# Kernel tuning notes

Hardware: AMD Instinct MI355X
Metric: run time of the kernel (lower is better)

## Reference

```python
import jax, jax.numpy as jnp
import numpy as np

INV_SQRT2 = np.float32(2.0 ** -0.5)
EPS = 1e-5


def _bn5(x, g, b, m, v):
    # inference-mode BatchNorm3d over channel axis 1 of NCDHW
    r = (1, -1, 1, 1, 1)
    return (x - m.reshape(r)) * (g.reshape(r) * jax.lax.rsqrt(v.reshape(r) + EPS)) + b.reshape(r)


def _conv3d(x, w, b, dil=1, pad=0):
    out = jax.lax.conv_general_dilated(
        x, w, window_strides=(1, 1, 1), padding=[(pad, pad)] * 3,
        rhs_dilation=(dil, dil, dil),
        dimension_numbers=('NCDHW', 'OIDHW', 'NCDHW'))
    return out + b.reshape(1, -1, 1, 1, 1)


def _haar_dwt2(x):
    # pywt dwt2(x, 'haar', axes=(-3,-2)) for even-length axes.
    # axis -3 (D): a = approx, d = detail (pywt sign: (x0 - x1)/sqrt2)
    a = (x[:, :, 0::2] + x[:, :, 1::2]) * INV_SQRT2
    d = (x[:, :, 0::2] - x[:, :, 1::2]) * INV_SQRT2
    # axis -2 (H)
    LL = (a[:, :, :, 0::2] + a[:, :, :, 1::2]) * INV_SQRT2  # 'aa'
    HL = (a[:, :, :, 0::2] - a[:, :, :, 1::2]) * INV_SQRT2  # 'ad'
    LH = (d[:, :, :, 0::2] + d[:, :, :, 1::2]) * INV_SQRT2  # 'da'
    HH = (d[:, :, :, 0::2] - d[:, :, :, 1::2]) * INV_SQRT2  # 'dd'
    return LL, LH, HL, HH


def setup_inputs() -> dict:
    key = jax.random.key(0)
    ks = jax.random.split(key, 12)
    B, C1, D, H, W = 2, 60, 128, 128, 64
    CH, R = 64, 4  # gate channels, CH // reduction_ratio
    f32 = jnp.float32
    inp = {
        'x1': jax.random.normal(ks[0], (B, C1, D // 2, H // 2, W), f32),
        'x2': jax.random.normal(ks[1], (B, 1, D, H, W), f32),
        # BatchNorm3d(4) on dwt features
        'bn_g': jnp.ones(4, f32), 'bn_b': jnp.zeros(4, f32),
        'bn_m': jnp.zeros(4, f32), 'bn_v': jnp.ones(4, f32),
        # BAM channel gate: Linear(64->4), BN1d(4), Linear(4->64)
        'cg_w1': jax.random.normal(ks[2], (R, CH), f32) * 0.05,
        'cg_b1': jnp.zeros(R, f32),
        'cg_bng': jnp.ones(R, f32), 'cg_bnb': jnp.zeros(R, f32),
        'cg_bnm': jnp.zeros(R, f32), 'cg_bnv': jnp.ones(R, f32),
        'cg_w2': jax.random.normal(ks[3], (CH, R), f32) * 0.05,
        'cg_b2': jnp.zeros(CH, f32),
        # BAM spatial gate
        'sg_w0': jax.random.normal(ks[4], (R, CH, 1, 1, 1), f32) * 0.05,
        'sg_b0': jnp.zeros(R, f32),
        'sg_g0': jnp.ones(R, f32), 'sg_be0': jnp.zeros(R, f32),
        'sg_m0': jnp.zeros(R, f32), 'sg_v0': jnp.ones(R, f32),
        'sg_w1': jax.random.normal(ks[5], (R, R, 3, 3, 3), f32) * 0.05,
        'sg_b1': jnp.zeros(R, f32),
        'sg_g1': jnp.ones(R, f32), 'sg_be1': jnp.zeros(R, f32),
        'sg_m1': jnp.zeros(R, f32), 'sg_v1': jnp.ones(R, f32),
        'sg_w2': jax.random.normal(ks[6], (R, R, 3, 3, 3), f32) * 0.05,
        'sg_b2': jnp.zeros(R, f32),
        'sg_g2': jnp.ones(R, f32), 'sg_be2': jnp.zeros(R, f32),
        'sg_m2': jnp.zeros(R, f32), 'sg_v2': jnp.ones(R, f32),
        'sg_w3': jax.random.normal(ks[7], (1, R, 1, 1, 1), f32) * 0.05,
        'sg_b3': jnp.zeros(1, f32),
    }
    return inp


def reference(x1, x2, bn_g, bn_b, bn_m, bn_v,
              cg_w1, cg_b1, cg_bng, cg_bnb, cg_bnm, cg_bnv, cg_w2, cg_b2,
              sg_w0, sg_b0, sg_g0, sg_be0, sg_m0, sg_v0,
              sg_w1, sg_b1, sg_g1, sg_be1, sg_m1, sg_v1,
              sg_w2, sg_b2, sg_g2, sg_be2, sg_m2, sg_v2,
              sg_w3, sg_b3):
    LL, LH, HL, HH = _haar_dwt2(x2)
    dwt = jnp.concatenate([LL, LH, HL, HH], axis=1)          # [B,4,D/2,H/2,W]
    dwt = jax.nn.relu(_bn5(dwt, bn_g, bn_b, bn_m, bn_v))
    feat = jnp.concatenate([dwt, x1], axis=1)                # [B,64,D/2,H/2,W]

    # BAM channel gate
    pooled = feat.mean(axis=(2, 3, 4))                        # [B,64]
    h = pooled @ cg_w1.T + cg_b1
    h = jax.nn.relu((h - cg_bnm) * (cg_bng * jax.lax.rsqrt(cg_bnv + EPS)) + cg_bnb)
    att_c = (h @ cg_w2.T + cg_b2)[:, :, None, None, None]     # [B,64,1,1,1]

    # BAM spatial gate
    s = jax.nn.relu(_bn5(_conv3d(feat, sg_w0, sg_b0), sg_g0, sg_be0, sg_m0, sg_v0))
    s = jax.nn.relu(_bn5(_conv3d(s, sg_w1, sg_b1, dil=4, pad=4), sg_g1, sg_be1, sg_m1, sg_v1))
    s = jax.nn.relu(_bn5(_conv3d(s, sg_w2, sg_b2, dil=4, pad=4), sg_g2, sg_be2, sg_m2, sg_v2))
    att_s = _conv3d(s, sg_w3, sg_b3)                          # [B,1,D/2,H/2,W]

    scale = 1.0 + jax.nn.sigmoid(att_c + att_s)
    return (feat * scale, LL)
```

## Files before the change

kernel.cpp:

```cpp
#include <hip/hip_runtime.h>
#include <math.h>

#define EPSBN 1e-5f

typedef float f32x2 __attribute__((ext_vector_type(2)));
typedef float f32x4 __attribute__((ext_vector_type(4)));

constexpr int B   = 2;
constexpr int C1  = 60;
constexpr int NV  = 64 * 64 * 64;
constexpr int NBa = NV / 512;

__global__ __launch_bounds__(256) void kA(
    const float* __restrict__ x1, const float* __restrict__ x2,
    const float* __restrict__ bn_g, const float* __restrict__ bn_b,
    const float* __restrict__ bn_m, const float* __restrict__ bn_v,
    const float* __restrict__ sg_w0, const float* __restrict__ sg_b0,
    const float* __restrict__ sg_g0, const float* __restrict__ sg_be0,
    const float* __restrict__ sg_m0, const float* __restrict__ sg_v0,
    float* __restrict__ dwtM, float* __restrict__ s0,
    float* __restrict__ part, float* __restrict__ outLL)
{
    __shared__ float wsumq[64][65];

    const int tid = threadIdx.x;
    const int qid = tid >> 2;

    float dsc[4], dsh[4], c0A[4], c0B[4];
    #pragma unroll
    for (int r = 0; r < 4; ++r) {
        float d = bn_g[r] * rsqrtf(bn_v[r] + EPSBN);
        dsc[r] = d; dsh[r] = bn_b[r] - bn_m[r] * d;
        float sc = sg_g0[r] * rsqrtf(sg_v0[r] + EPSBN);
        c0A[r] = sc; c0B[r] = (sg_b0[r] - sg_m0[r]) * sc + sg_be0[r];
    }

    const int b = blockIdx.y;
    const int v = blockIdx.x * 512 + tid * 2;
    const int x = v & 63, y = (v >> 6) & 63, z = v >> 12;

    const float* px2 = x2 + (size_t)b * (128 * 128 * 64);
    const size_t i00 = ((size_t)(2 * z) * 128 + 2 * y) * 64 + x;
    const float2 p00 = *(const float2*)(px2 + i00);
    const float2 p01 = *(const float2*)(px2 + i00 + 64);
    const float2 p10 = *(const float2*)(px2 + i00 + 8192);
    const float2 p11 = *(const float2*)(px2 + i00 + 8256);
    const float* q00 = (const float*)&p00; const float* q01 = (const float*)&p01;
    const float* q10 = (const float*)&p10; const float* q11 = (const float*)&p11;

    float tv[2][4], llv[2];
    #pragma unroll
    for (int vi = 0; vi < 2; ++vi) {
        float a = q00[vi], bb = q01[vi], c = q10[vi], d = q11[vi];
        float LL = 0.5f * (a + bb + c + d);
        float LH = 0.5f * (a + bb - c - d);
        float HL = 0.5f * (a - bb + c - d);
        float HH = 0.5f * (a - bb - c + d);
        llv[vi] = LL;
        tv[vi][0] = fmaxf(LL * dsc[0] + dsh[0], 0.f);
        tv[vi][1] = fmaxf(LH * dsc[1] + dsh[1], 0.f);
        tv[vi][2] = fmaxf(HL * dsc[2] + dsh[2], 0.f);
        tv[vi][3] = fmaxf(HH * dsc[3] + dsh[3], 0.f);
    }
    {
        f32x2 ll2 = { llv[0], llv[1] };
        __builtin_nontemporal_store(ll2, (f32x2*)(outLL + (size_t)b * NV + v));
    }

    float acc[2][4] = {};
    #pragma unroll
    for (int c = 0; c < 4; ++c) {
        #pragma unroll
        for (int vi = 0; vi < 2; ++vi) {
            float t = tv[vi][c];
            #pragma unroll
            for (int r = 0; r < 4; ++r) acc[vi][r] += sg_w0[r * 64 + c] * t;
        }
        float rs = tv[0][c] + tv[1][c];
        rs += __shfl_xor(rs, 1);
        rs += __shfl_xor(rs, 2);
        if ((tid & 3) == 0) wsumq[c][qid] = rs;
        *(float2*)(dwtM + ((size_t)b * 4 + c) * NV + v) = make_float2(tv[0][c], tv[1][c]);
    }

    const float* px1 = x1 + (size_t)b * C1 * NV + v;
    #pragma unroll 2
    for (int c = 0; c < C1; ++c) {
        const float2 f = *(const float2*)(px1 + (size_t)c * NV);
        #pragma unroll
        for (int r = 0; r < 4; ++r) {
            const float w = sg_w0[r * 64 + 4 + c];
            acc[0][r] += w * f.x;
            acc[1][r] += w * f.y;
        }
        float rs = f.x + f.y;
        rs += __shfl_xor(rs, 1);
        rs += __shfl_xor(rs, 2);
        if ((tid & 3) == 0) wsumq[4 + c][qid] = rs;
    }

    float4* ps0 = (float4*)s0 + (size_t)b * NV + v;
    #pragma unroll
    for (int vi = 0; vi < 2; ++vi)
        ps0[vi] = make_float4(fmaxf(acc[vi][0] * c0A[0] + c0B[0], 0.f),
                              fmaxf(acc[vi][1] * c0A[1] + c0B[1], 0.f),
                              fmaxf(acc[vi][2] * c0A[2] + c0B[2], 0.f),
                              fmaxf(acc[vi][3] * c0A[3] + c0B[3], 0.f));

    __syncthreads();
    if (tid < 64) {
        const float* rowp = &wsumq[tid][0];
        float p = 0.f;
        #pragma unroll
        for (int i = 0; i < 64; ++i) p += rowp[i];
        part[((size_t)b * 64 + tid) * NBa + blockIdx.x] = p;
    }
}

__global__ __launch_bounds__(256) void kConv1(
    const float* __restrict__ sin_,
    const float* __restrict__ w, const float* __restrict__ bias,
    const float* __restrict__ g, const float* __restrict__ be,
    const float* __restrict__ m, const float* __restrict__ vv,
    const float* __restrict__ part,
    const float* __restrict__ cg_w1, const float* __restrict__ cg_b1,
    const float* __restrict__ cg_bng, const float* __restrict__ cg_bnb,
    const float* __restrict__ cg_bnm, const float* __restrict__ cg_bnv,
    const float* __restrict__ cg_w2, const float* __restrict__ cg_b2,
    float* __restrict__ ec,
    float* __restrict__ outp)
{
    const int tid = threadIdx.x;
    const int b = blockIdx.y;

    if (blockIdx.x == NBa) {
        __shared__ float pooled[64];
        __shared__ float h[4];
        const int c = tid >> 2, q = tid & 3;
        const float4* pp = (const float4*)(part + ((size_t)b * 64 + c) * NBa + q * 128);
        float sm = 0.f;
        #pragma unroll
        for (int i = 0; i < 32; ++i) { float4 f = pp[i]; sm += f.x + f.y + f.z + f.w; }
        sm += __shfl_xor(sm, 1);
        sm += __shfl_xor(sm, 2);
        if (q == 0) pooled[c] = sm * (1.0f / NV);
        __syncthreads();
        if (tid < 4) {
            float a = cg_b1[tid];
            for (int cc = 0; cc < 64; ++cc) a += pooled[cc] * cg_w1[tid * 64 + cc];
            float sc = cg_bng[tid] * rsqrtf(cg_bnv[tid] + EPSBN);
            h[tid] = fmaxf((a - cg_bnm[tid]) * sc + cg_bnb[tid], 0.f);
        }
        __syncthreads();
        if (tid < 64) {
            float a = cg_b2[tid];
            #pragma unroll
            for (int r = 0; r < 4; ++r) a += h[r] * cg_w2[tid * 4 + r];
            ec[b * 64 + tid] = __expf(-a);
        }
        return;
    }

    __shared__ float4 wl4[108];
    if (tid < 108) {
        const int t = tid >> 2, r = tid & 3;
        wl4[tid] = make_float4(w[r * 108 +      t], w[r * 108 +  27 + t],
                               w[r * 108 + 54 + t], w[r * 108 +  81 + t]);
    }
    float cAr[4], cBr[4];
    #pragma unroll
    for (int r = 0; r < 4; ++r) {
        float sc = g[r] * rsqrtf(vv[r] + EPSBN);
        cAr[r] = sc;
        cBr[r] = (bias[r] - m[r]) * sc + be[r];
    }
    __syncthreads();

    const int v = blockIdx.x * 512 + tid * 2;
    const int x = v & 63, y = (v >> 6) & 63, z = v >> 12;
    const float4* pin = (const float4*)sin_ + (size_t)b * NV;

    float acc[2][4] = {};
    #pragma unroll
    for (int kz = -1; kz <= 1; ++kz) {
        const int zz = z + 4 * kz;
        if ((unsigned)zz >= 64u) continue;
        #pragma unroll
        for (int ky = -1; ky <= 1; ++ky) {
            const int yy = y + 4 * ky;
            if ((unsigned)yy >= 64u) continue;
            #pragma unroll
            for (int kx = -1; kx <= 1; ++kx) {
                const int xx = x + 4 * kx;
                if ((unsigned)xx >= 64u) continue;
                const int t = (kz + 1) * 9 + (ky + 1) * 3 + (kx + 1);
                const int vt = zz * 4096 + yy * 64 + xx;
                const float4 w0 = wl4[t * 4 + 0];
                const float4 w1 = wl4[t * 4 + 1];
                const float4 w2 = wl4[t * 4 + 2];
                const float4 w3 = wl4[t * 4 + 3];
                #pragma unroll
                for (int vi = 0; vi < 2; ++vi) {
                    const float4 tap = pin[vt + vi];
                    acc[vi][0] += w0.x * tap.x + w0.y * tap.y + w0.z * tap.z + w0.w * tap.w;
                    acc[vi][1] += w1.x * tap.x + w1.y * tap.y + w1.z * tap.z + w1.w * tap.w;
                    acc[vi][2] += w2.x * tap.x + w2.y * tap.y + w2.z * tap.z + w2.w * tap.w;
                    acc[vi][3] += w3.x * tap.x + w3.y * tap.y + w3.z * tap.z + w3.w * tap.w;
                }
            }
        }
    }

    float4* po = (float4*)outp + (size_t)b * NV + v;
    #pragma unroll
    for (int vi = 0; vi < 2; ++vi)
        po[vi] = make_float4(fmaxf(acc[vi][0] * cAr[0] + cBr[0], 0.f),
                             fmaxf(acc[vi][1] * cAr[1] + cBr[1], 0.f),
                             fmaxf(acc[vi][2] * cAr[2] + cBr[2], 0.f),
                             fmaxf(acc[vi][3] * cAr[3] + cBr[3], 0.f));
}

__global__ __launch_bounds__(256) void kMulF(
    const float* __restrict__ x1,
    const float* __restrict__ dwtM,
    const float* __restrict__ s1,
    const float* __restrict__ w, const float* __restrict__ bias,
    const float* __restrict__ g, const float* __restrict__ be,
    const float* __restrict__ m, const float* __restrict__ vv,
    const float* __restrict__ w3, const float* __restrict__ b3,
    const float* __restrict__ ec,
    float* __restrict__ out0)
{
    const int tid = threadIdx.x;
    const int b = blockIdx.x >> 9;
    const int blockBase = (blockIdx.x & 511) * 128;

    __shared__ float4 wl4[108];
    __shared__ float ecs[64];
    if (tid < 108) {
        const int t = tid >> 2, r = tid & 3;
        wl4[tid] = make_float4(w[r * 108 +      t], w[r * 108 +  27 + t],
                               w[r * 108 + 54 + t], w[r * 108 +  81 + t]);
    }
    if (tid < 64) ecs[tid] = ec[b * 64 + tid];
    float cAr[4], cBr[4], w3l[4];
    #pragma unroll
    for (int r = 0; r < 4; ++r) {
        float sc = g[r] * rsqrtf(vv[r] + EPSBN);
        cAr[r] = sc;
        cBr[r] = (bias[r] - m[r]) * sc + be[r];
        w3l[r] = w3[r];
    }
    const float b3l = b3[0];
    __syncthreads();

    const int vq = blockBase + (tid & 127);
    const int v  = vq * 4;
    const int x0 = v & 63, y = (v >> 6) & 63, z = v >> 12;
    const int ch0 = (tid >> 7) * 32;

    const float4* pin = (const float4*)s1 + (size_t)b * NV;
    float acc[4][4] = {};
    #pragma unroll
    for (int kz = -1; kz <= 1; ++kz) {
        const int zz = z + 4 * kz;
        if ((unsigned)zz >= 64u) continue;
        #pragma unroll
        for (int ky = -1; ky <= 1; ++ky) {
            const int yy = y + 4 * ky;
            if ((unsigned)yy >= 64u) continue;
            #pragma unroll
            for (int kx = -1; kx <= 1; ++kx) {
                const int xb = x0 + 4 * kx;
                if ((unsigned)xb >= 64u) continue;
                const int t = (kz + 1) * 9 + (ky + 1) * 3 + (kx + 1);
                const int vt = zz * 4096 + yy * 64 + xb;
                const float4 w0 = wl4[t * 4 + 0];
                const float4 w1 = wl4[t * 4 + 1];
                const float4 w2 = wl4[t * 4 + 2];
                const float4 w3q = wl4[t * 4 + 3];
                #pragma unroll
                for (int vi = 0; vi < 4; ++vi) {
                    const float4 tap = pin[vt + vi];
                    acc[vi][0] += w0.x * tap.x + w0.y * tap.y + w0.z * tap.z + w0.w * tap.w;
                    acc[vi][1] += w1.x * tap.x + w1.y * tap.y + w1.z * tap.z + w1.w * tap.w;
                    acc[vi][2] += w2.x * tap.x + w2.y * tap.y + w2.z * tap.z + w2.w * tap.w;
                    acc[vi][3] += w3q.x * tap.x + w3q.y * tap.y + w3q.z * tap.z + w3q.w * tap.w;
                }
            }
        }
    }

    float es[4];
    #pragma unroll
    for (int vi = 0; vi < 4; ++vi) {
        float r0 = fmaxf(acc[vi][0] * cAr[0] + cBr[0], 0.f);
        float r1 = fmaxf(acc[vi][1] * cAr[1] + cBr[1], 0.f);
        float r2 = fmaxf(acc[vi][2] * cAr[2] + cBr[2], 0.f);
        float r3 = fmaxf(acc[vi][3] * cAr[3] + cBr[3], 0.f);
        es[vi] = __expf(-(b3l + w3l[0] * r0 + w3l[1] * r1 + w3l[2] * r2 + w3l[3] * r3));
    }

    float* po = out0 + ((size_t)b * 64 + ch0) * NV + v;
    #pragma unroll 4
    for (int cc = 0; cc < 32; ++cc) {
        const int c = ch0 + cc;
        const float* basep = (c < 4)
            ? dwtM + ((size_t)b * 4 + c) * NV
            : x1   + ((size_t)b * C1 + (c - 4)) * NV;
        const float4 in4 = *(const float4*)(basep + v);
        const float e = ecs[c];
        f32x4 o;
        o.x = in4.x * (1.f + __builtin_amdgcn_rcpf(1.f + e * es[0]));
        o.y = in4.y * (1.f + __builtin_amdgcn_rcpf(1.f + e * es[1]));
        o.z = in4.z * (1.f + __builtin_amdgcn_rcpf(1.f + e * es[2]));
        o.w = in4.w * (1.f + __builtin_amdgcn_rcpf(1.f + e * es[3]));
        __builtin_nontemporal_store(o, (f32x4*)(po + (size_t)cc * NV));
    }
}

extern "C" void kernel_launch(void* const* d_in, const int* in_sizes, int n_in,
                              void* d_out, int out_size, void* d_ws, size_t ws_size,
                              hipStream_t stream)
{
    const float* x1 = (const float*)d_in[0];
    const float* x2 = (const float*)d_in[1];
    const float* bn_g = (const float*)d_in[2];
    const float* bn_b = (const float*)d_in[3];
    const float* bn_m = (const float*)d_in[4];
    const float* bn_v = (const float*)d_in[5];
    const float* cg_w1 = (const float*)d_in[6];
    const float* cg_b1 = (const float*)d_in[7];
    const float* cg_bng = (const float*)d_in[8];
    const float* cg_bnb = (const float*)d_in[9];
    const float* cg_bnm = (const float*)d_in[10];
    const float* cg_bnv = (const float*)d_in[11];
    const float* cg_w2 = (const float*)d_in[12];
    const float* cg_b2 = (const float*)d_in[13];
    const float* sg_w0 = (const float*)d_in[14];
    const float* sg_b0 = (const float*)d_in[15];
    const float* sg_g0 = (const float*)d_in[16];
    const float* sg_be0 = (const float*)d_in[17];
    const float* sg_m0 = (const float*)d_in[18];
    const float* sg_v0 = (const float*)d_in[19];
    const float* sg_w1 = (const float*)d_in[20];
    const float* sg_b1 = (const float*)d_in[21];
    const float* sg_g1 = (const float*)d_in[22];
    const float* sg_be1 = (const float*)d_in[23];
    const float* sg_m1 = (const float*)d_in[24];
    const float* sg_v1 = (const float*)d_in[25];
    const float* sg_w2 = (const float*)d_in[26];
    const float* sg_b2 = (const float*)d_in[27];
    const float* sg_g2 = (const float*)d_in[28];
    const float* sg_be2 = (const float*)d_in[29];
    const float* sg_m2 = (const float*)d_in[30];
    const float* sg_v2 = (const float*)d_in[31];
    const float* sg_w3 = (const float*)d_in[32];
    const float* sg_b3 = (const float*)d_in[33];

    float* ws = (float*)d_ws;
    float* dwtM = ws;
    float* s0   = ws + 2097152;
    float* s1   = ws + 4194304;
    float* part = ws + 6291456;
    float* ec   = ws + 6356992;

    float* out0  = (float*)d_out;
    float* outLL = out0 + (size_t)B * 64 * NV;

    dim3 blk(256);
    kA<<<dim3(NBa, B), blk, 0, stream>>>(x1, x2, bn_g, bn_b, bn_m, bn_v,
                                         sg_w0, sg_b0, sg_g0, sg_be0, sg_m0, sg_v0,
                                         dwtM, s0, part, outLL);
    kConv1<<<dim3(NBa + 1, B), blk, 0, stream>>>(s0, sg_w1, sg_b1, sg_g1, sg_be1, sg_m1, sg_v1,
                                                 part, cg_w1, cg_b1, cg_bng, cg_bnb, cg_bnm, cg_bnv,
                                                 cg_w2, cg_b2, ec, s1);
    kMulF<<<dim3(1024), blk, 0, stream>>>(x1, dwtM, s1, sg_w2, sg_b2, sg_g2, sg_be2, sg_m2, sg_v2,
                                          sg_w3, sg_b3, ec, out0);
}
```

Baseline: 112.3 us.

## Compute kMulF spatial conv once per voxel via LDS and widen kA vectors

In the final kernel, the dilated 3x3x3 conv and sigmoid-gate term were computed twice per voxel, once by each of the two thread halves handling different channel groups. Now every thread computes the conv for two voxels, writes the gate terms into a 512-entry shared buffer, and after a barrier all threads read them for the channel-scaling loop. Separately, kA now handles four voxels per thread with float4 loads and stores, halving its block count; the partial-sum layout and the channel-gate reduction in kConv1 are adjusted to match. The cost is an extra barrier and shared-memory traffic in kMulF, and higher register pressure in kA.

```diff
diff --git a/kernel.cpp b/kernel.cpp
--- a/kernel.cpp
+++ b/kernel.cpp
@@ -9,7 +9,8 @@
 constexpr int B   = 2;
 constexpr int C1  = 60;
 constexpr int NV  = 64 * 64 * 64;
-constexpr int NBa = NV / 512;
+constexpr int NBa = NV / 1024;
+constexpr int NBc = NV / 512;
 
 __global__ __launch_bounds__(256) void kA(
     const float* __restrict__ x1, const float* __restrict__ x2,
@@ -36,21 +37,21 @@
     }
 
     const int b = blockIdx.y;
-    const int v = blockIdx.x * 512 + tid * 2;
+    const int v = blockIdx.x * 1024 + tid * 4;
     const int x = v & 63, y = (v >> 6) & 63, z = v >> 12;
 
     const float* px2 = x2 + (size_t)b * (128 * 128 * 64);
     const size_t i00 = ((size_t)(2 * z) * 128 + 2 * y) * 64 + x;
-    const float2 p00 = *(const float2*)(px2 + i00);
-    const float2 p01 = *(const float2*)(px2 + i00 + 64);
-    const float2 p10 = *(const float2*)(px2 + i00 + 8192);
-    const float2 p11 = *(const float2*)(px2 + i00 + 8256);
+    const float4 p00 = *(const float4*)(px2 + i00);
+    const float4 p01 = *(const float4*)(px2 + i00 + 64);
+    const float4 p10 = *(const float4*)(px2 + i00 + 8192);
+    const float4 p11 = *(const float4*)(px2 + i00 + 8256);
     const float* q00 = (const float*)&p00; const float* q01 = (const float*)&p01;
     const float* q10 = (const float*)&p10; const float* q11 = (const float*)&p11;
 
-    float tv[2][4], llv[2];
-    #pragma unroll
-    for (int vi = 0; vi < 2; ++vi) {
+    float tv[4][4], llv[4];
+    #pragma unroll
+    for (int vi = 0; vi < 4; ++vi) {
         float a = q00[vi], bb = q01[vi], c = q10[vi], d = q11[vi];
         float LL = 0.5f * (a + bb + c + d);
         float LH = 0.5f * (a + bb - c - d);
@@ -63,37 +64,39 @@
         tv[vi][3] = fmaxf(HH * dsc[3] + dsh[3], 0.f);
     }
     {
-        f32x2 ll2 = { llv[0], llv[1] };
-        __builtin_nontemporal_store(ll2, (f32x2*)(outLL + (size_t)b * NV + v));
-    }
-
-    float acc[2][4] = {};
+        f32x4 ll4 = { llv[0], llv[1], llv[2], llv[3] };
+        __builtin_nontemporal_store(ll4, (f32x4*)(outLL + (size_t)b * NV + v));
+    }
+
+    float acc[4][4] = {};
     #pragma unroll
     for (int c = 0; c < 4; ++c) {
         #pragma unroll
-        for (int vi = 0; vi < 2; ++vi) {
+        for (int vi = 0; vi < 4; ++vi) {
             float t = tv[vi][c];
             #pragma unroll
             for (int r = 0; r < 4; ++r) acc[vi][r] += sg_w0[r * 64 + c] * t;
         }
-        float rs = tv[0][c] + tv[1][c];
+        float rs = tv[0][c] + tv[1][c] + tv[2][c] + tv[3][c];
         rs += __shfl_xor(rs, 1);
         rs += __shfl_xor(rs, 2);
         if ((tid & 3) == 0) wsumq[c][qid] = rs;
-        *(float2*)(dwtM + ((size_t)b * 4 + c) * NV + v) = make_float2(tv[0][c], tv[1][c]);
+        *(float4*)(dwtM + ((size_t)b * 4 + c) * NV + v) =
+            make_float4(tv[0][c], tv[1][c], tv[2][c], tv[3][c]);
     }
 
     const float* px1 = x1 + (size_t)b * C1 * NV + v;
     #pragma unroll 2
     for (int c = 0; c < C1; ++c) {
-        const float2 f = *(const float2*)(px1 + (size_t)c * NV);
+        const float4 f = *(const float4*)(px1 + (size_t)c * NV);
+        const float* fv = (const float*)&f;
         #pragma unroll
         for (int r = 0; r < 4; ++r) {
             const float w = sg_w0[r * 64 + 4 + c];
-            acc[0][r] += w * f.x;
-            acc[1][r] += w * f.y;
-        }
-        float rs = f.x + f.y;
+            #pragma unroll
+            for (int vi = 0; vi < 4; ++vi) acc[vi][r] += w * fv[vi];
+        }
+        float rs = f.x + f.y + f.z + f.w;
         rs += __shfl_xor(rs, 1);
         rs += __shfl_xor(rs, 2);
         if ((tid & 3) == 0) wsumq[4 + c][qid] = rs;
@@ -101,7 +104,7 @@
 
     float4* ps0 = (float4*)s0 + (size_t)b * NV + v;
     #pragma unroll
-    for (int vi = 0; vi < 2; ++vi)
+    for (int vi = 0; vi < 4; ++vi)
         ps0[vi] = make_float4(fmaxf(acc[vi][0] * c0A[0] + c0B[0], 0.f),
                               fmaxf(acc[vi][1] * c0A[1] + c0B[1], 0.f),
                               fmaxf(acc[vi][2] * c0A[2] + c0B[2], 0.f),
@@ -133,14 +136,14 @@
     const int tid = threadIdx.x;
     const int b = blockIdx.y;
 
-    if (blockIdx.x == NBa) {
+    if (blockIdx.x == NBc) {
         __shared__ float pooled[64];
         __shared__ float h[4];
         const int c = tid >> 2, q = tid & 3;
-        const float4* pp = (const float4*)(part + ((size_t)b * 64 + c) * NBa + q * 128);
+        const float4* pp = (const float4*)(part + ((size_t)b * 64 + c) * NBa + q * 64);
         float sm = 0.f;
         #pragma unroll
-        for (int i = 0; i < 32; ++i) { float4 f = pp[i]; sm += f.x + f.y + f.z + f.w; }
+        for (int i = 0; i < 16; ++i) { float4 f = pp[i]; sm += f.x + f.y + f.z + f.w; }
         sm += __shfl_xor(sm, 1);
         sm += __shfl_xor(sm, 2);
         if (q == 0) pooled[c] = sm * (1.0f / NV);
@@ -233,10 +236,11 @@
 {
     const int tid = threadIdx.x;
     const int b = blockIdx.x >> 9;
-    const int blockBase = (blockIdx.x & 511) * 128;
+    const int vb = (blockIdx.x & 511) * 512;
 
     __shared__ float4 wl4[108];
     __shared__ float ecs[64];
+    __shared__ float esb[512];
     if (tid < 108) {
         const int t = tid >> 2, r = tid & 3;
         wl4[tid] = make_float4(w[r * 108 +      t], w[r * 108 +  27 + t],
@@ -254,52 +258,57 @@
     const float b3l = b3[0];
     __syncthreads();
 
-    const int vq = blockBase + (tid & 127);
-    const int v  = vq * 4;
-    const int x0 = v & 63, y = (v >> 6) & 63, z = v >> 12;
-    const int ch0 = (tid >> 7) * 32;
-
-    const float4* pin = (const float4*)s1 + (size_t)b * NV;
-    float acc[4][4] = {};
-    #pragma unroll
-    for (int kz = -1; kz <= 1; ++kz) {
-        const int zz = z + 4 * kz;
-        if ((unsigned)zz >= 64u) continue;
-        #pragma unroll
-        for (int ky = -1; ky <= 1; ++ky) {
-            const int yy = y + 4 * ky;
-            if ((unsigned)yy >= 64u) continue;
-            #pragma unroll
-            for (int kx = -1; kx <= 1; ++kx) {
-                const int xb = x0 + 4 * kx;
-                if ((unsigned)xb >= 64u) continue;
-                const int t = (kz + 1) * 9 + (ky + 1) * 3 + (kx + 1);
-                const int vt = zz * 4096 + yy * 64 + xb;
-                const float4 w0 = wl4[t * 4 + 0];
-                const float4 w1 = wl4[t * 4 + 1];
-                const float4 w2 = wl4[t * 4 + 2];
-                const float4 w3q = wl4[t * 4 + 3];
+    {
+        const int v = vb + tid * 2;
+        const int x = v & 63, y = (v >> 6) & 63, z = v >> 12;
+        const float4* pin = (const float4*)s1 + (size_t)b * NV;
+        float acc[2][4] = {};
+        #pragma unroll
+        for (int kz = -1; kz <= 1; ++kz) {
+            const int zz = z + 4 * kz;
+            if ((unsigned)zz >= 64u) continue;
+            #pragma unroll
+            for (int ky = -1; ky <= 1; ++ky) {
+                const int yy = y + 4 * ky;
+                if ((unsigned)yy >= 64u) continue;
                 #pragma unroll
-                for (int vi = 0; vi < 4; ++vi) {
-                    const float4 tap = pin[vt + vi];
-                    acc[vi][0] += w0.x * tap.x + w0.y * tap.y + w0.z * tap.z + w0.w * tap.w;
-                    acc[vi][1] += w1.x * tap.x + w1.y * tap.y + w1.z * tap.z + w1.w * tap.w;
-                    acc[vi][2] += w2.x * tap.x + w2.y * tap.y + w2.z * tap.z + w2.w * tap.w;
-                    acc[vi][3] += w3q.x * tap.x + w3q.y * tap.y + w3q.z * tap.z + w3q.w * tap.w;
+                for (int kx = -1; kx <= 1; ++kx) {
+                    const int xx = x + 4 * kx;
+                    if ((unsigned)xx >= 64u) continue;
+                    const int t = (kz + 1) * 9 + (ky + 1) * 3 + (kx + 1);
+                    const int vt = zz * 4096 + yy * 64 + xx;
+                    const float4 w0 = wl4[t * 4 + 0];
+                    const float4 w1 = wl4[t * 4 + 1];
+                    const float4 w2 = wl4[t * 4 + 2];
+                    const float4 w3q = wl4[t * 4 + 3];
+                    #pragma unroll
+                    for (int vi = 0; vi < 2; ++vi) {
+                        const float4 tap = pin[vt + vi];
+                        acc[vi][0] += w0.x * tap.x + w0.y * tap.y + w0.z * tap.z + w0.w * tap.w;
+                        acc[vi][1] += w1.x * tap.x + w1.y * tap.y + w1.z * tap.z + w1.w * tap.w;
+                        acc[vi][2] += w2.x * tap.x + w2.y * tap.y + w2.z * tap.z + w2.w * tap.w;
+                        acc[vi][3] += w3q.x * tap.x + w3q.y * tap.y + w3q.z * tap.z + w3q.w * tap.w;
+                    }
                 }
             }
         }
-    }
-
-    float es[4];
-    #pragma unroll
-    for (int vi = 0; vi < 4; ++vi) {
-        float r0 = fmaxf(acc[vi][0] * cAr[0] + cBr[0], 0.f);
-        float r1 = fmaxf(acc[vi][1] * cAr[1] + cBr[1], 0.f);
-        float r2 = fmaxf(acc[vi][2] * cAr[2] + cBr[2], 0.f);
-        float r3 = fmaxf(acc[vi][3] * cAr[3] + cBr[3], 0.f);
-        es[vi] = __expf(-(b3l + w3l[0] * r0 + w3l[1] * r1 + w3l[2] * r2 + w3l[3] * r3));
-    }
+        #pragma unroll
+        for (int vi = 0; vi < 2; ++vi) {
+            float r0 = fmaxf(acc[vi][0] * cAr[0] + cBr[0], 0.f);
+            float r1 = fmaxf(acc[vi][1] * cAr[1] + cBr[1], 0.f);
+            float r2 = fmaxf(acc[vi][2] * cAr[2] + cBr[2], 0.f);
+            float r3 = fmaxf(acc[vi][3] * cAr[3] + cBr[3], 0.f);
+            esb[tid * 2 + vi] =
+                __expf(-(b3l + w3l[0] * r0 + w3l[1] * r1 + w3l[2] * r2 + w3l[3] * r3));
+        }
+    }
+    __syncthreads();
+
+    const int q = tid & 127;
+    const int v = vb + q * 4;
+    const int ch0 = (tid >> 7) * 32;
+    const float es0 = esb[q * 4 + 0], es1 = esb[q * 4 + 1];
+    const float es2 = esb[q * 4 + 2], es3 = esb[q * 4 + 3];
 
     float* po = out0 + ((size_t)b * 64 + ch0) * NV + v;
     #pragma unroll 4
@@ -311,10 +320,10 @@
         const float4 in4 = *(const float4*)(basep + v);
         const float e = ecs[c];
         f32x4 o;
-        o.x = in4.x * (1.f + __builtin_amdgcn_rcpf(1.f + e * es[0]));
-        o.y = in4.y * (1.f + __builtin_amdgcn_rcpf(1.f + e * es[1]));
-        o.z = in4.z * (1.f + __builtin_amdgcn_rcpf(1.f + e * es[2]));
-        o.w = in4.w * (1.f + __builtin_amdgcn_rcpf(1.f + e * es[3]));
+        o.x = in4.x * (1.f + __builtin_amdgcn_rcpf(1.f + e * es0));
+        o.y = in4.y * (1.f + __builtin_amdgcn_rcpf(1.f + e * es1));
+        o.z = in4.z * (1.f + __builtin_amdgcn_rcpf(1.f + e * es2));
+        o.w = in4.w * (1.f + __builtin_amdgcn_rcpf(1.f + e * es3));
         __builtin_nontemporal_store(o, (f32x4*)(po + (size_t)cc * NV));
     }
 }
@@ -363,7 +372,7 @@
     float* s0   = ws + 2097152;
     float* s1   = ws + 4194304;
     float* part = ws + 6291456;
-    float* ec   = ws + 6356992;
+    float* ec   = ws + 6324224;
 
     float* out0  = (float*)d_out;
     float* outLL = out0 + (size_t)B * 64 * NV;
@@ -372,7 +381,7 @@
     kA<<<dim3(NBa, B), blk, 0, stream>>>(x1, x2, bn_g, bn_b, bn_m, bn_v,
                                          sg_w0, sg_b0, sg_g0, sg_be0, sg_m0, sg_v0,
                                          dwtM, s0, part, outLL);
-    kConv1<<<dim3(NBa + 1, B), blk, 0, stream>>>(s0, sg_w1, sg_b1, sg_g1, sg_be1, sg_m1, sg_v1,
+    kConv1<<<dim3(NBc + 1, B), blk, 0, stream>>>(s0, sg_w1, sg_b1, sg_g1, sg_be1, sg_m1, sg_v1,
                                                  part, cg_w1, cg_b1, cg_bng, cg_bnb, cg_bnm, cg_bnv,
                                                  cg_w2, cg_b2, ec, s1);
     kMulF<<<dim3(1024), blk, 0, stream>>>(x1, dwtM, s1, sg_w2, sg_b2, sg_g2, sg_be2, sg_m2, sg_v2,
```

After: 100.3 us. -10.7%, faster.
